# Optimization experiments

Hardware: AMD Instinct MI355X
Metric: run time of the kernel (lower is better)

## Reference

```python
import jax, jax.numpy as jnp
import numpy as np
import math

B, IN, OUT = 32, 8192, 8192
DENSITY = 0.15

def _inverse_softplus(v):
    return math.log(math.expm1(v))

def setup_inputs() -> dict:
    key = jax.random.key(0)
    k1, k2, k3, k4 = jax.random.split(key, 4)
    inputs = jax.random.normal(k1, (B, IN), dtype=jnp.float32)
    active = jax.random.uniform(k2, (OUT, IN)) < DENSITY
    sign = jnp.where(jax.random.uniform(k3, (OUT, IN)) < 0.5, 1, -1)
    weight_state = jnp.where(active, sign, 0).astype(jnp.int32)
    # log_scale initialized so softplus(log_scale) = 1/sqrt(in_features)
    log_scale = jnp.full((OUT,), _inverse_softplus(1.0 / math.sqrt(IN)), dtype=jnp.float32)
    bias = jax.random.normal(k4, (OUT,), dtype=jnp.float32) * 0.01
    return {"inputs": inputs, "log_scale": log_scale, "bias": bias, "weight_state": weight_state}

def reference(inputs, log_scale, bias, weight_state):
    # scale = softplus(log_scale).clamp_min(1e-4), per output channel
    scale = jnp.maximum(jax.nn.softplus(log_scale), 1e-4)  # [OUT]
    # effective_weight = ternary_state * scale[:, None]; out = x @ W^T + b
    w = weight_state.astype(inputs.dtype) * scale[:, None]  # [OUT, IN]
    return jnp.einsum('bi,oi->bo', inputs, w) + bias
```

## Files before the change

kernel.cpp:

```cpp
#include <hip/hip_runtime.h>
#include <hip/hip_bf16.h>
#include <cmath>


#define K_SZ   8192
#define N_SZ   8192
#define B_SZ   32
#define KSPLIT 4
#define KB_TOT (K_SZ / 32)
#define KB_PER (KB_TOT / KSPLIT)

typedef __attribute__((ext_vector_type(8))) short bf16x8;
typedef __attribute__((ext_vector_type(4))) float f32x4;

__device__ __forceinline__ unsigned pack_rn(float lo, float hi) {
  unsigned ul = __builtin_bit_cast(unsigned, lo) + 0x8000u;
  unsigned uh = __builtin_bit_cast(unsigned, hi) + 0x8000u;
  return (ul >> 16) | (uh & 0xFFFF0000u);
}
__device__ __forceinline__ unsigned pack_w(int w0, int w1) {
  unsigned u0 = __builtin_bit_cast(unsigned, (float)w0);
  unsigned u1 = __builtin_bit_cast(unsigned, (float)w1);
  return (u0 >> 16) | (u1 & 0xFFFF0000u);
}

__global__ void xprep(const float* __restrict__ X, uint4* __restrict__ Xr) {
  int t = blockIdx.x * blockDim.x + threadIdx.x;
  int lane = t & 63;
  int chunk = t >> 6;
  int kb = chunk >> 1;
  int mt = chunk & 1;
  int row = mt * 16 + (lane & 15);
  int k0 = kb * 32 + (lane >> 4) * 8;
  const float* p = X + (size_t)row * K_SZ + k0;
  float4 a = *(const float4*)p;
  float4 b = *(const float4*)(p + 4);
  uint4 o;
  o.x = pack_rn(a.x, a.y); o.y = pack_rn(a.z, a.w);
  o.z = pack_rn(b.x, b.y); o.w = pack_rn(b.z, b.w);
  Xr[t] = o;
}

__global__ __launch_bounds__(256, 2) void tmm(
    const int*   __restrict__ W,
    const uint4* __restrict__ Xr,
    const float* __restrict__ log_scale,
    const float* __restrict__ bias,
    float*       __restrict__ out) {
  const int tid  = threadIdx.x;
  const int w    = tid >> 6;
  const int lane = tid & 63;
  const int r    = lane & 15;
  const int q    = lane >> 4;
  const int ntg  = blockIdx.x * 4 + w;
  const int o0   = ntg * 16;
  const int kb0  = blockIdx.y * KB_PER;
  const int kbEnd = kb0 + KB_PER;

  const int*   gW = W + (size_t)(o0 + r) * K_SZ + q * 8;
  const uint4* xA = Xr + lane;

  f32x4 acc0 = {0.f, 0.f, 0.f, 0.f};
  f32x4 acc1 = {0.f, 0.f, 0.f, 0.f};

  int4  wa0, wa1, wb0, wb1, wc0, wc1, wd0, wd1;
  uint4 xa0, xa1, xb0, xb1, xc0, xc1, xd0, xd1;

#define LDW(kb, lo, hi) { const int* g_ = gW + (size_t)(kb) * 32; \
    lo = *(const int4*)g_; hi = *(const int4*)(g_ + 4); }
#define LDA(kb, m0, m1) { const uint4* x_ = xA + (size_t)(kb) * 128; \
    m0 = x_[0]; m1 = x_[64]; }
#define COMP(lo, hi, m0, m1) { \
    union { unsigned u[4]; bf16x8 v; } Bf_; \
    Bf_.u[0] = pack_w(lo.x, lo.y); Bf_.u[1] = pack_w(lo.z, lo.w); \
    Bf_.u[2] = pack_w(hi.x, hi.y); Bf_.u[3] = pack_w(hi.z, hi.w); \
    acc0 = __builtin_amdgcn_mfma_f32_16x16x32_bf16( \
        __builtin_bit_cast(bf16x8, m0), Bf_.v, acc0, 0, 0, 0); \
    acc1 = __builtin_amdgcn_mfma_f32_16x16x32_bf16( \
        __builtin_bit_cast(bf16x8, m1), Bf_.v, acc1, 0, 0, 0); }

  LDW(kb0 + 0, wa0, wa1); LDW(kb0 + 1, wb0, wb1);
  LDA(kb0 + 0, xa0, xa1); LDA(kb0 + 1, xb0, xb1);

  for (int kb = kb0; kb < kbEnd; kb += 4) {
    LDW(kb + 2, wc0, wc1); LDW(kb + 3, wd0, wd1);
    LDA(kb + 2, xc0, xc1); LDA(kb + 3, xd0, xd1);
    COMP(wa0, wa1, xa0, xa1);
    COMP(wb0, wb1, xb0, xb1);
    int k4 = kb + 4 < kbEnd ? kb + 4 : kb0;
    int k5 = kb + 5 < kbEnd ? kb + 5 : kb0;
    LDW(k4, wa0, wa1); LDW(k5, wb0, wb1);
    LDA(k4, xa0, xa1); LDA(k5, xb0, xb1);
    COMP(wc0, wc1, xc0, xc1);
    COMP(wd0, wd1, xd0, xd1);
  }

  const int o = o0 + r;
  float sp    = log1pf(expf(log_scale[o]));
  float scale = fmaxf(sp, 1e-4f);
  float badd  = (blockIdx.y == 0) ? bias[o] : 0.f;
  #pragma unroll
  for (int rg = 0; rg < 4; ++rg) {
    atomicAdd(&out[(size_t)(q * 4 + rg) * N_SZ + o],      acc0[rg] * scale + badd);
    atomicAdd(&out[(size_t)(16 + q * 4 + rg) * N_SZ + o], acc1[rg] * scale + badd);
  }
#undef LDW
#undef LDA
#undef COMP
}

extern "C" void kernel_launch(void* const* d_in, const int* in_sizes, int n_in,
                              void* d_out, int out_size, void* d_ws, size_t ws_size,
                              hipStream_t stream) {
  const float* X  = (const float*)d_in[0];
  const float* ls = (const float*)d_in[1];
  const float* bs = (const float*)d_in[2];
  const int*   W  = (const int*)d_in[3];
  float* out = (float*)d_out;
  uint4* Xr = (uint4*)d_ws;

  hipMemsetAsync(out, 0, (size_t)B_SZ * N_SZ * sizeof(float), stream);
  xprep<<<128, 256, 0, stream>>>(X, Xr);
  dim3 grid(N_SZ / 64, KSPLIT);
  tmm<<<grid, 256, 0, stream>>>(W, Xr, ls, bs, out);
}
```

Measured before the change: 395.0 us.

## Stage weight tiles through LDS with coalesced row loads and smaller N tiles

Weight rows are now read with fully coalesced 512-byte row segments into a padded LDS tile, then each wave reads its 16x32 fragments from LDS. Each block covers 32 outputs and the 4 waves split work over M and N tiles, so every wave handles one M tile. The goal is to improve DRAM access efficiency on the 256MB int32 weight stream. In exchange it adds two barriers per step and LDS traffic, and halves per-wave MFMA work.

```diff
diff --git a/kernel.cpp b/kernel.cpp
--- a/kernel.cpp
+++ b/kernel.cpp
@@ -7,8 +7,11 @@
 #define N_SZ   8192
 #define B_SZ   32
 #define KSPLIT 4
-#define KB_TOT (K_SZ / 32)
-#define KB_PER (KB_TOT / KSPLIT)
+#define KCH    (K_SZ / KSPLIT)
+#define BN     32
+#define BK     128
+#define STEPS  (KCH / BK)
+#define LDW    132
 
 typedef __attribute__((ext_vector_type(8))) short bf16x8;
 typedef __attribute__((ext_vector_type(4))) float f32x4;
@@ -41,72 +44,91 @@
   Xr[t] = o;
 }
 
-__global__ __launch_bounds__(256, 2) void tmm(
+__global__ __launch_bounds__(256, 4) void tmm(
     const int*   __restrict__ W,
     const uint4* __restrict__ Xr,
     const float* __restrict__ log_scale,
     const float* __restrict__ bias,
     float*       __restrict__ out) {
+  __shared__ int lds[32 * LDW];
+
   const int tid  = threadIdx.x;
   const int w    = tid >> 6;
   const int lane = tid & 63;
+  const int q    = lane >> 4;
   const int r    = lane & 15;
-  const int q    = lane >> 4;
-  const int ntg  = blockIdx.x * 4 + w;
-  const int o0   = ntg * 16;
-  const int kb0  = blockIdx.y * KB_PER;
-  const int kbEnd = kb0 + KB_PER;
+  const int nb   = blockIdx.x * BN;
+  const int kh   = blockIdx.y;
+  const int mt   = w & 1;
+  const int nt   = w >> 1;
 
-  const int*   gW = W + (size_t)(o0 + r) * K_SZ + q * 8;
-  const uint4* xA = Xr + lane;
+  const int srow = 8 * w + (lane >> 5);
+  const int skof = 4 * (lane & 31);
+  const int* gW = W + (size_t)(nb + srow) * K_SZ + (size_t)kh * KCH + skof;
+  const int lof = srow * LDW + skof;
 
-  f32x4 acc0 = {0.f, 0.f, 0.f, 0.f};
-  f32x4 acc1 = {0.f, 0.f, 0.f, 0.f};
+  int4 wr0 = *(const int4*)(gW + 0 * 2 * K_SZ);
+  int4 wr1 = *(const int4*)(gW + 1 * 2 * K_SZ);
+  int4 wr2 = *(const int4*)(gW + 2 * 2 * K_SZ);
+  int4 wr3 = *(const int4*)(gW + 3 * 2 * K_SZ);
 
-  int4  wa0, wa1, wb0, wb1, wc0, wc1, wd0, wd1;
-  uint4 xa0, xa1, xb0, xb1, xc0, xc1, xd0, xd1;
+  const uint4* xr = Xr + lane;
+  const int kbb = kh * (KCH / 32);
+  uint4 a0 = xr[(size_t)((kbb + 0) * 2 + mt) * 64];
+  uint4 a1 = xr[(size_t)((kbb + 1) * 2 + mt) * 64];
+  uint4 a2 = xr[(size_t)((kbb + 2) * 2 + mt) * 64];
+  uint4 a3 = xr[(size_t)((kbb + 3) * 2 + mt) * 64];
 
-#define LDW(kb, lo, hi) { const int* g_ = gW + (size_t)(kb) * 32; \
-    lo = *(const int4*)g_; hi = *(const int4*)(g_ + 4); }
-#define LDA(kb, m0, m1) { const uint4* x_ = xA + (size_t)(kb) * 128; \
-    m0 = x_[0]; m1 = x_[64]; }
-#define COMP(lo, hi, m0, m1) { \
-    union { unsigned u[4]; bf16x8 v; } Bf_; \
-    Bf_.u[0] = pack_w(lo.x, lo.y); Bf_.u[1] = pack_w(lo.z, lo.w); \
-    Bf_.u[2] = pack_w(hi.x, hi.y); Bf_.u[3] = pack_w(hi.z, hi.w); \
-    acc0 = __builtin_amdgcn_mfma_f32_16x16x32_bf16( \
-        __builtin_bit_cast(bf16x8, m0), Bf_.v, acc0, 0, 0, 0); \
-    acc1 = __builtin_amdgcn_mfma_f32_16x16x32_bf16( \
-        __builtin_bit_cast(bf16x8, m1), Bf_.v, acc1, 0, 0, 0); }
+  f32x4 acc = {0.f, 0.f, 0.f, 0.f};
+  const int Rbase = (nt * 16 + r) * LDW;
 
-  LDW(kb0 + 0, wa0, wa1); LDW(kb0 + 1, wb0, wb1);
-  LDA(kb0 + 0, xa0, xa1); LDA(kb0 + 1, xb0, xb1);
+  for (int step = 0; step < STEPS; ++step) {
+    __syncthreads();
+    *(int4*)&lds[lof + 0 * 2 * LDW] = wr0;
+    *(int4*)&lds[lof + 1 * 2 * LDW] = wr1;
+    *(int4*)&lds[lof + 2 * 2 * LDW] = wr2;
+    *(int4*)&lds[lof + 3 * 2 * LDW] = wr3;
+    if (step + 1 < STEPS) {
+      const int* g = gW + (step + 1) * BK;
+      wr0 = *(const int4*)(g + 0 * 2 * K_SZ);
+      wr1 = *(const int4*)(g + 1 * 2 * K_SZ);
+      wr2 = *(const int4*)(g + 2 * 2 * K_SZ);
+      wr3 = *(const int4*)(g + 3 * 2 * K_SZ);
+    }
+    __syncthreads();
 
-  for (int kb = kb0; kb < kbEnd; kb += 4) {
-    LDW(kb + 2, wc0, wc1); LDW(kb + 3, wd0, wd1);
-    LDA(kb + 2, xc0, xc1); LDA(kb + 3, xd0, xd1);
-    COMP(wa0, wa1, xa0, xa1);
-    COMP(wb0, wb1, xb0, xb1);
-    int k4 = kb + 4 < kbEnd ? kb + 4 : kb0;
-    int k5 = kb + 5 < kbEnd ? kb + 5 : kb0;
-    LDW(k4, wa0, wa1); LDW(k5, wb0, wb1);
-    LDA(k4, xa0, xa1); LDA(k5, xb0, xb1);
-    COMP(wc0, wc1, xc0, xc1);
-    COMP(wd0, wd1, xd0, xd1);
+    uint4 ca0 = a0, ca1 = a1, ca2 = a2, ca3 = a3;
+    if (step + 1 < STEPS) {
+      int kb2 = kbb + (step + 1) * 4;
+      a0 = xr[(size_t)((kb2 + 0) * 2 + mt) * 64];
+      a1 = xr[(size_t)((kb2 + 1) * 2 + mt) * 64];
+      a2 = xr[(size_t)((kb2 + 2) * 2 + mt) * 64];
+      a3 = xr[(size_t)((kb2 + 3) * 2 + mt) * 64];
+    }
+
+    #pragma unroll
+    for (int s = 0; s < 4; ++s) {
+      uint4 ca = (s == 0) ? ca0 : (s == 1) ? ca1 : (s == 2) ? ca2 : ca3;
+      int ro = Rbase + s * 32 + q * 8;
+      int4 b0 = *(const int4*)&lds[ro];
+      int4 b1 = *(const int4*)&lds[ro + 4];
+      union { unsigned u[4]; bf16x8 v; } Bf;
+      Bf.u[0] = pack_w(b0.x, b0.y); Bf.u[1] = pack_w(b0.z, b0.w);
+      Bf.u[2] = pack_w(b1.x, b1.y); Bf.u[3] = pack_w(b1.z, b1.w);
+      bf16x8 Af = __builtin_bit_cast(bf16x8, ca);
+      acc = __builtin_amdgcn_mfma_f32_16x16x32_bf16(Af, Bf.v, acc, 0, 0, 0);
+    }
   }
 
-  const int o = o0 + r;
+  const int o = nb + nt * 16 + r;
   float sp    = log1pf(expf(log_scale[o]));
   float scale = fmaxf(sp, 1e-4f);
-  float badd  = (blockIdx.y == 0) ? bias[o] : 0.f;
+  float badd  = (kh == 0) ? bias[o] : 0.f;
   #pragma unroll
   for (int rg = 0; rg < 4; ++rg) {
-    atomicAdd(&out[(size_t)(q * 4 + rg) * N_SZ + o],      acc0[rg] * scale + badd);
-    atomicAdd(&out[(size_t)(16 + q * 4 + rg) * N_SZ + o], acc1[rg] * scale + badd);
+    int b = mt * 16 + q * 4 + rg;
+    atomicAdd(&out[(size_t)b * N_SZ + o], acc[rg] * scale + badd);
   }
-#undef LDW
-#undef LDA
-#undef COMP
 }
 
 extern "C" void kernel_launch(void* const* d_in, const int* in_sizes, int n_in,
@@ -119,8 +141,8 @@
   float* out = (float*)d_out;
   uint4* Xr = (uint4*)d_ws;
 
-  hipMemsetAsync(out, 0, (size_t)B_SZ * N_SZ * sizeof(float), stream);
+  (void)hipMemsetAsync(out, 0, (size_t)B_SZ * N_SZ * sizeof(float), stream);
   xprep<<<128, 256, 0, stream>>>(X, Xr);
-  dim3 grid(N_SZ / 64, KSPLIT);
+  dim3 grid(N_SZ / BN, KSPLIT);
   tmm<<<grid, 256, 0, stream>>>(W, Xr, ls, bs, out);
 }
```

New measurement: 369.9 us. -6.4%, faster.
